# Optimization experiments

Measured on AMD Instinct MI355X. Metric: run time of the kernel, lower is better.

Reference implementation:

```python
import jax, jax.numpy as jnp
import numpy as np

Q = 4          # num_quantizers
K = 2048       # codebook_size
D = 256        # dim
B, N = 8, 8192 # batch, tokens (N % Q == 0)


def l2norm(t, eps=1e-12):
    return t / jnp.maximum(jnp.linalg.norm(t, axis=-1, keepdims=True), eps)


def setup_inputs() -> dict:
    key = jax.random.key(0)
    kx, ke = jax.random.split(key)
    x = jax.random.normal(kx, (B, N, D), dtype=jnp.float32)
    embed = jax.random.normal(ke, (Q, K, D), dtype=jnp.float32)
    return {"x": x, "embed": embed}


def reference(x, embed):
    b, n, d = x.shape
    q = embed.shape[0]
    m = n // q  # tokens per quantizer chunk
    # chunk along token axis (dim=1), as torch.chunk(x, Q, dim=1)
    xc = x.reshape(b, q, m, d).transpose(1, 0, 2, 3)  # [Q, B, M, D]

    def one_vq(xq, eq):
        # xq: [B, M, D], eq: [K, D]
        xn = l2norm(xq)
        en = l2norm(eq)
        dist = jnp.einsum('bmd,kd->bmk', xn, en)   # cosine similarity
        ind = jnp.argmax(dist, axis=-1)            # temp=0 gumbel -> argmax
        quant = eq[ind]                            # F.embedding with raw embed
        return quant, ind

    quant_c, ind_c = jax.vmap(one_vq)(xc, embed)   # [Q,B,M,D], [Q,B,M]
    quantized = quant_c.transpose(1, 0, 2, 3).reshape(b, n, d)
    encoding = ind_c.transpose(1, 0, 2).reshape(b, n)
    # eval mode: loss is sum of Q zero tensors of shape [1]
    vq_loss = jnp.zeros((1,), dtype=x.dtype)
    return quantized, encoding, vq_loss
```

## Files before the change

kernel.cpp:

```cpp
#include <hip/hip_runtime.h>
#include <math.h>

#define Bq 8
#define Nq 8192
#define Dq 256
#define Qq 4
#define Kq 2048
#define Mq (Nq / Qq)
#define TT (Bq * Nq)
#define QUANT_ELEMS ((size_t)TT * Dq)

#define CAP1Q 4096
#define THRESH 3e-4f
#define CAND_MAX 16

#define WS_CNT_OFF    0u
#define WS_LIST_OFF   1024u
#define WS_SX_OFF     66560u
#define WS_ENH_OFF    1377280u
#define WS_ENP_OFF    5571584u
#define WS_PART_OFF   13960192u

typedef __attribute__((ext_vector_type(8))) _Float16 f16x8;
typedef __attribute__((ext_vector_type(4))) _Float16 f16x4;
typedef __attribute__((ext_vector_type(4))) float    f32x4;

__device__ __forceinline__ void async_load16(const void* g, void* s) {
    __builtin_amdgcn_global_load_lds(
        (const __attribute__((address_space(1))) void*)g,
        (__attribute__((address_space(3))) void*)s, 16, 0, 0);
}

__device__ __forceinline__ float f32_div(float a, float b) {
    return (float)((double)a / (double)b);
}

__device__ __forceinline__ float np_norm_wave(const float* __restrict__ src, int ln) {
#pragma clang fp contract(off)
    float r = 0.0f;
    if (ln < 16) {
        const float* p = src + (ln >> 3) * 128 + (ln & 7);
        #pragma unroll
        for (int m = 0; m < 16; ++m) { float v = p[m * 8]; r = r + v * v; }
    }
    float t = r + __shfl_xor(r, 1, 64);
    t = t + __shfl_xor(t, 2, 64);
    t = t + __shfl_xor(t, 4, 64);
    float b0 = __shfl(t, 0, 64);
    float b1 = __shfl(t, 8, 64);
    float n2 = b0 + b1;
    return fmaxf((float)sqrt((double)n2), 1e-12f);
}

__global__ __launch_bounds__(256) void prep_kernel(const float* __restrict__ embed,
                                                   const float* __restrict__ x,
                                                   char* __restrict__ enh,
                                                   float* __restrict__ enp,
                                                   float* __restrict__ sxa,
                                                   int* __restrict__ cnt,
                                                   float* __restrict__ out) {
    if (blockIdx.x >= 2048) {
        const int tid = threadIdx.x;
        const int qd  = tid & 3;
        const int row = (blockIdx.x - 2048) * 64 + (tid >> 2);
        const float* xr = x + (size_t)row * Dq + qd * 8;
        float s2 = 0.f;
        #pragma unroll
        for (int ch = 0; ch < 8; ++ch) {
            float4 u = *(const float4*)(xr + ch * 32);
            float4 v = *(const float4*)(xr + ch * 32 + 4);
            s2 += u.x * u.x + u.y * u.y + u.z * u.z + u.w * u.w;
            s2 += v.x * v.x + v.y * v.y + v.z * v.z + v.w * v.w;
        }
        s2 += __shfl_xor(s2, 1, 64);
        s2 += __shfl_xor(s2, 2, 64);
        float sxv = 1.0f / fmaxf(sqrtf(s2), 1e-12f);
        if (qd == 0) sxa[row] = sxv;
        return;
    }

    if (blockIdx.x == 0) {
        if (threadIdx.x < 4) cnt[threadIdx.x] = 0;
        if (threadIdx.x == 0) out[QUANT_ELEMS + TT] = 0.0f;
    }

    int row = blockIdx.x * 4 + (threadIdx.x >> 6);
    int ln  = threadIdx.x & 63;
    const float* src = embed + (size_t)row * Dq;

    float4 v = *(const float4*)(src + ln * 4);
    float s = v.x * v.x + v.y * v.y + v.z * v.z + v.w * v.w;
    #pragma unroll
    for (int m = 1; m < 64; m <<= 1) s += __shfl_xor(s, m, 64);
    float sx = 1.0f / fmaxf(sqrtf(s), 1e-12f);
    int q = row >> 11, k = row & 2047, Tb = k >> 5, c = k & 31;
    int g = ln >> 1, h = ln & 1;
    f16x4 o;
    o[0] = (_Float16)(v.x * sx); o[1] = (_Float16)(v.y * sx);
    o[2] = (_Float16)(v.z * sx); o[3] = (_Float16)(v.w * sx);
    char* dst = enh + ((size_t)(q * 64 + Tb)) * 16384 + c * 512 + ((g ^ c) << 4) + h * 8;
    *(f16x4*)dst = o;

    float nm = np_norm_wave(src, ln);
    float* dstp = enp + (size_t)row * Dq;
    #pragma unroll
    for (int e = 0; e < 4; ++e) dstp[ln * 4 + e] = f32_div(src[ln * 4 + e], nm);
}

__global__ __launch_bounds__(256, 2) void gemm_kernel(const float* __restrict__ x,
                                                      const float* __restrict__ sxa,
                                                      const char* __restrict__ enh,
                                                      float4* __restrict__ part) {
    __shared__ __align__(16) char es[3][16384];

    const int tid = threadIdx.x;
    const int wv  = tid >> 6;
    const int ln  = tid & 63;
    const int qd  = ln >> 4;
    const int l15 = ln & 15;

    const int bid = blockIdx.x;
    const int h   = bid & 1;
    const int g   = bid >> 1;
    const int b   = g >> 5;
    const int rem = g & 31;
    const int q   = rem >> 3;
    const int m0  = (rem & 7) << 8;
    const int t0  = b * Nq + q * Mq + m0;
    const int t0w = t0 + wv * 64;

    f16x8 ah[4][8];
    #pragma unroll
    for (int mf = 0; mf < 4; ++mf) {
        const int tok = t0w + mf * 16 + l15;
        const float sxv = sxa[tok];
        const float* xr = x + (size_t)tok * Dq + qd * 8;
        #pragma unroll
        for (int ch = 0; ch < 8; ++ch) {
            float4 u = *(const float4*)(xr + ch * 32);
            float4 v = *(const float4*)(xr + ch * 32 + 4);
            f16x8 f;
            f[0] = (_Float16)(u.x * sxv); f[1] = (_Float16)(u.y * sxv);
            f[2] = (_Float16)(u.z * sxv); f[3] = (_Float16)(u.w * sxv);
            f[4] = (_Float16)(v.x * sxv); f[5] = (_Float16)(v.y * sxv);
            f[6] = (_Float16)(v.z * sxv); f[7] = (_Float16)(v.w * sxv);
            ah[mf][ch] = f;
        }
    }

    const char* ebase = enh + ((size_t)(q * 64 + h * 32)) * 16384;
    const int off0 = wv * 1024 + ln * 16;

    __builtin_amdgcn_sched_barrier(0);
    asm volatile("s_waitcnt vmcnt(0)");
    __builtin_amdgcn_sched_barrier(0);
    #pragma unroll
    for (int i = 0; i < 4; ++i)
        async_load16(ebase + i * 4096 + off0, es[0] + i * 4096 + off0);
    #pragma unroll
    for (int i = 0; i < 4; ++i)
        async_load16(ebase + 16384 + i * 4096 + off0, es[1] + i * 4096 + off0);
    __builtin_amdgcn_sched_barrier(0);

    float b1[4][4], b2[4][4];
    int   ic[4][4];
    #pragma unroll
    for (int mf = 0; mf < 4; ++mf)
        #pragma unroll
        for (int r = 0; r < 4; ++r) { b1[mf][r] = -2.0f; b2[mf][r] = -2.0f; ic[mf][r] = 0; }

    int rb = 0;
    for (int T = 0; T < 32; ++T) {
        if (T < 31) asm volatile("s_waitcnt vmcnt(4)");
        else        asm volatile("s_waitcnt vmcnt(0)");
        __builtin_amdgcn_sched_barrier(0);
        __builtin_amdgcn_s_barrier();
        __builtin_amdgcn_sched_barrier(0);

        if (T + 2 < 32) {
            int wb = rb + 2; if (wb >= 3) wb -= 3;
            const char* src = ebase + (size_t)(T + 2) * 16384;
            #pragma unroll
            for (int i = 0; i < 4; ++i)
                async_load16(src + i * 4096 + off0, es[wb] + i * 4096 + off0);
        }
        __builtin_amdgcn_sched_barrier(0);

        const char* esb = es[rb];

        #pragma unroll
        for (int s = 0; s < 2; ++s) {
            const int  c  = s * 16 + l15;
            const char* cb = esb + c * 512;
            f16x8 bfr[8];
            #pragma unroll
            for (int ch = 0; ch < 8; ++ch)
                bfr[ch] = *(const f16x8*)(cb + ((((ch << 2) | qd) ^ c) << 4));

            f32x4 a[4];
            #pragma unroll
            for (int mf = 0; mf < 4; ++mf) a[mf] = (f32x4){0.f, 0.f, 0.f, 0.f};
            #pragma unroll
            for (int ch = 0; ch < 8; ++ch) {
                #pragma unroll
                for (int mf = 0; mf < 4; ++mf)
                    a[mf] = __builtin_amdgcn_mfma_f32_16x16x32_f16(ah[mf][ch], bfr[ch], a[mf], 0, 0, 0);
            }

            const int cg = (h << 10) | (T << 5) | (s << 4) | l15;
            #pragma unroll
            for (int mf = 0; mf < 4; ++mf)
                #pragma unroll
                for (int r = 0; r < 4; ++r) {
                    float sv = a[mf][r];
                    bool  gt = sv > b1[mf][r];
                    b2[mf][r] = __builtin_amdgcn_fmed3f(sv, b1[mf][r], b2[mf][r]);
                    b1[mf][r] = fmaxf(b1[mf][r], sv);
                    ic[mf][r] = gt ? cg : ic[mf][r];
                }
        }
        if (++rb == 3) rb = 0;
    }

    float fb1[4][4], fb2[4][4];
    int   fic[4][4];
    #pragma unroll
    for (int mf = 0; mf < 4; ++mf)
        #pragma unroll
        for (int r = 0; r < 4; ++r) {
            float v1 = b1[mf][r], v2 = b2[mf][r]; int vi = ic[mf][r];
            #pragma unroll
            for (int m = 1; m < 16; m <<= 1) {
                float o1 = __shfl_xor(v1, m, 64);
                float o2 = __shfl_xor(v2, m, 64);
                int   oi = __shfl_xor(vi, m, 64);
                if (o1 > v1 || (o1 == v1 && oi < vi)) { v2 = fmaxf(v1, o2); v1 = o1; vi = oi; }
                else v2 = fmaxf(v2, o1);
            }
            fb1[mf][r] = v1; fb2[mf][r] = v2; fic[mf][r] = vi;
        }

    if (l15 == 0) {
        #pragma unroll
        for (int mf = 0; mf < 4; ++mf)
            #pragma unroll
            for (int r = 0; r < 4; ++r) {
                int t = t0w + mf * 16 + qd * 4 + r;
                float4 pv;
                pv.x = fb1[mf][r];
                pv.y = fb2[mf][r];
                pv.z = __int_as_float(fic[mf][r]);
                pv.w = 0.f;
                part[(size_t)h * TT + t] = pv;
            }
    }
}

__global__ __launch_bounds__(256) void merge_kernel(const float* __restrict__ embed,
                                                    const float4* __restrict__ part,
                                                    float* __restrict__ out,
                                                    int* __restrict__ cnt,
                                                    int* __restrict__ list) {
    const int wv = threadIdx.x >> 6, ln = threadIdx.x & 63;
    const int nw = gridDim.x * 4;

    for (int t = blockIdx.x * 4 + wv; t < TT; t += nw) {
        float4 pa = part[t];
        float4 pb = part[TT + t];
        float v1, v2; int vi;
        if (pb.x > pa.x) { v1 = pb.x; vi = __float_as_int(pb.z); v2 = fmaxf(pa.x, pb.y); }
        else             { v1 = pa.x; vi = __float_as_int(pa.z); v2 = fmaxf(pb.x, pa.y); }
        const int q = (t >> 11) & 3;

        int inlist = 0;
        if (ln == 0) {
            if (v1 - v2 < THRESH) {
                int pos = atomicAdd(&cnt[q], 1);
                if (pos < CAP1Q) { list[q * CAP1Q + pos] = t; inlist = 1; }
            }
            if (!inlist) out[QUANT_ELEMS + (size_t)t] = (float)vi;
        }
        inlist = __shfl(inlist, 0, 64);
        if (!inlist) {
            const float* er = embed + ((size_t)(q * Kq + vi)) * Dq;
            float4 v = *(const float4*)(er + ln * 4);
            *(float4*)(out + (size_t)t * Dq + ln * 4) = v;
        }
    }
}

__global__ __launch_bounds__(256) void cand_kernel(const float* __restrict__ x,
                                                   const float* __restrict__ sxa,
                                                   const char* __restrict__ enh,
                                                   const float* __restrict__ enp,
                                                   const float4* __restrict__ part,
                                                   const float* __restrict__ embed,
                                                   const int* __restrict__ cnt,
                                                   const int* __restrict__ list,
                                                   float* __restrict__ out) {
#pragma clang fp contract(off)
    __shared__ float xn[16][Dq];
    __shared__ int   stok[16];
    __shared__ float sv1[16];
    __shared__ int   scnt[16];
    __shared__ unsigned short scand[16][CAND_MAX];
    __shared__ float sc_s[256];
    __shared__ int   sc_c[256];
    __shared__ int   fbc[16];

    const int tid = threadIdx.x;
    const int wv  = tid >> 6;
    const int ln  = tid & 63;
    const int qd  = ln >> 4;
    const int l15 = ln & 15;

    int cq[4], nbq[4], total = 0;
    #pragma unroll
    for (int q = 0; q < 4; ++q) {
        int c = cnt[q]; if (c > CAP1Q) c = CAP1Q;
        cq[q] = c; nbq[q] = (c + 15) >> 4; total += nbq[q];
    }

    for (int j = blockIdx.x; j < total; j += gridDim.x) {
        int rem = j, q = 0;
        while (rem >= nbq[q]) { rem -= nbq[q]; ++q; }
        const int base = rem << 4;

        if (tid < 16) {
            int idx = base + tid;
            int tok = list[q * CAP1Q + (idx < cq[q] ? idx : base)];
            stok[tid] = tok;
            scnt[tid] = 0;
            sv1[tid]  = fmaxf(part[tok].x, part[TT + tok].x);
        }
        __syncthreads();

        f16x8 ah[8];
        {
            const int tok = stok[l15];
            const float sxv = sxa[tok];
            const float* xr = x + (size_t)tok * Dq + qd * 8;
            #pragma unroll
            for (int ch = 0; ch < 8; ++ch) {
                float4 u = *(const float4*)(xr + ch * 32);
                float4 v = *(const float4*)(xr + ch * 32 + 4);
                f16x8 f;
                f[0] = (_Float16)(u.x * sxv); f[1] = (_Float16)(u.y * sxv);
                f[2] = (_Float16)(u.z * sxv); f[3] = (_Float16)(u.w * sxv);
                f[4] = (_Float16)(v.x * sxv); f[5] = (_Float16)(v.y * sxv);
                f[6] = (_Float16)(v.z * sxv); f[7] = (_Float16)(v.w * sxv);
                ah[ch] = f;
            }
        }
        float thr[4];
        #pragma unroll
        for (int r = 0; r < 4; ++r) thr[r] = sv1[qd * 4 + r] - THRESH;

        const char* qbase = enh + ((size_t)(q * 64)) * 16384;
        for (int tt = 0; tt < 16; ++tt) {
            const int T = wv * 16 + tt;
            const char* tb = qbase + (size_t)T * 16384;
            #pragma unroll
            for (int s = 0; s < 2; ++s) {
                const int  c  = s * 16 + l15;
                const char* cb = tb + c * 512;
                f16x8 bfr[8];
                #pragma unroll
                for (int ch = 0; ch < 8; ++ch)
                    bfr[ch] = *(const f16x8*)(cb + ((((ch << 2) | qd) ^ c) << 4));

                f32x4 a = {0.f, 0.f, 0.f, 0.f};
                #pragma unroll
                for (int ch = 0; ch < 8; ++ch)
                    a = __builtin_amdgcn_mfma_f32_16x16x32_f16(ah[ch], bfr[ch], a, 0, 0, 0);

                const int cg = (T << 5) | (s << 4) | l15;
                #pragma unroll
                for (int r = 0; r < 4; ++r) {
                    if (a[r] >= thr[r]) {
                        int slot = qd * 4 + r;
                        int pos = atomicAdd(&scnt[slot], 1);
                        if (pos < CAND_MAX) scand[slot][pos] = (unsigned short)cg;
                    }
                }
            }
        }
        __syncthreads();

        for (int rr = 0; rr < 4; ++rr) {
            int i = wv * 4 + rr;
            const float* xr = x + (size_t)stok[i] * Dq;
            float nm = np_norm_wave(xr, ln);
            #pragma unroll
            for (int e = 0; e < 4; ++e)
                xn[i][ln * 4 + e] = f32_div(xr[ln * 4 + e], nm);
        }
        __syncthreads();

        {
            const int i = tid >> 4, sl = tid & 15;
            const int nc = scnt[i];
            float bs = -2.0f; int bc = 0x7fffffff;
            if (nc <= CAND_MAX && sl < nc) {
                int code = scand[i][sl];
                const float* er2 = enp + ((size_t)(q * Kq + code)) * Dq;
                float l0 = 0.f, l1 = 0.f, l2 = 0.f, l3 = 0.f;
                for (int d = 0; d < Dq; d += 4) {
                    float4 e = *(const float4*)(er2 + d);
                    float4 xv = *(const float4*)&xn[i][d];
                    l0 = l0 + xv.x * e.x; l1 = l1 + xv.y * e.y;
                    l2 = l2 + xv.z * e.z; l3 = l3 + xv.w * e.w;
                }
                bs = (l0 + l1) + (l2 + l3);
                bc = code;
            }
            sc_s[tid] = bs; sc_c[tid] = bc;
        }
        __syncthreads();
        if (tid < 16) {
            float bs = sc_s[tid * 16]; int bc = sc_c[tid * 16];
            #pragma unroll
            for (int sl = 1; sl < 16; ++sl) {
                float os = sc_s[tid * 16 + sl]; int oc = sc_c[tid * 16 + sl];
                if (os > bs || (os == bs && oc < bc)) { bs = os; bc = oc; }
            }
            fbc[tid] = bc;
        }
        __syncthreads();

        for (int i = 0; i < 16; ++i) {
            if (scnt[i] > CAND_MAX) {
                float bs = -2.0f; int bc = 0x7fffffff;
                for (int k = 0; k < 8; ++k) {
                    int code = k * 256 + tid;
                    const float* er2 = enp + ((size_t)(q * Kq + code)) * Dq;
                    float l0 = 0.f, l1 = 0.f, l2 = 0.f, l3 = 0.f;
                    for (int d = 0; d < Dq; d += 4) {
                        float4 e = *(const float4*)(er2 + d);
                        float4 xv = *(const float4*)&xn[i][d];
                        l0 = l0 + xv.x * e.x; l1 = l1 + xv.y * e.y;
                        l2 = l2 + xv.z * e.z; l3 = l3 + xv.w * e.w;
                    }
                    float sE = (l0 + l1) + (l2 + l3);
                    if (sE > bs || (sE == bs && code < bc)) { bs = sE; bc = code; }
                }
                sc_s[tid] = bs; sc_c[tid] = bc;
                __syncthreads();
                if (tid == 0) {
                    for (int t2 = 1; t2 < 256; ++t2) {
                        float os = sc_s[t2]; int oc = sc_c[t2];
                        if (os > bs || (os == bs && oc < bc)) { bs = os; bc = oc; }
                    }
                    fbc[i] = bc;
                }
                __syncthreads();
            }
        }

        for (int rr = 0; rr < 4; ++rr) {
            const int i = wv * 4 + rr;
            const int tok = stok[i];
            const int bc = fbc[i];
            if (ln == 0) out[QUANT_ELEMS + (size_t)tok] = (float)bc;
            const float* er = embed + ((size_t)(q * Kq + bc)) * Dq;
            float4 v = *(const float4*)(er + ln * 4);
            *(float4*)(out + (size_t)tok * Dq + ln * 4) = v;
        }
        __syncthreads();
    }
}

extern "C" void kernel_launch(void* const* d_in, const int* in_sizes, int n_in,
                              void* d_out, int out_size, void* d_ws, size_t ws_size,
                              hipStream_t stream) {
    const float* x     = (const float*)d_in[0];
    const float* embed = (const float*)d_in[1];
    float* out = (float*)d_out;
    char*  ws  = (char*)d_ws;
    int*    cnt    = (int*)(ws + WS_CNT_OFF);
    int*    list   = (int*)(ws + WS_LIST_OFF);
    float*  sxa    = (float*)(ws + WS_SX_OFF);
    char*   enh    = ws + WS_ENH_OFF;
    float*  enp    = (float*)(ws + WS_ENP_OFF);
    float4* part   = (float4*)(ws + WS_PART_OFF);

    prep_kernel<<<3072, 256, 0, stream>>>(embed, x, enh, enp, sxa, cnt, out);
    gemm_kernel<<<512, 256, 0, stream>>>(x, sxa, enh, part);
    merge_kernel<<<2048, 256, 0, stream>>>(embed, part, out, cnt, list);
    cand_kernel<<<1024, 256, 0, stream>>>(x, sxa, enh, enp, part, embed, cnt, list, out);
}
```

Before: 279.4 us.

## Give each wave private double-buffered codebook staging to drop block barriers

Replaces the block-shared triple-buffered LDS ring, which needed an s_barrier every iteration, with per-wave private double buffers. Each wave now loads its own full copy of every 16-code half-tile. This removes inter-wave synchronization, but every wave issues the global loads for all codes, so global traffic into LDS is four times higher. LDS use grows from 48KB to 64KB per block, which may limit occupancy at two blocks per CU.

New measurement: 285.1 us. 2.0% more time.

```diff
diff --git a/kernel.cpp b/kernel.cpp
--- a/kernel.cpp
+++ b/kernel.cpp
@@ -111,7 +111,7 @@
                                                       const float* __restrict__ sxa,
                                                       const char* __restrict__ enh,
                                                       float4* __restrict__ part) {
-    __shared__ __align__(16) char es[3][16384];
+    __shared__ __align__(16) char es[4][2][8192];
 
     const int tid = threadIdx.x;
     const int wv  = tid >> 6;
@@ -149,18 +149,17 @@
     }
 
     const char* ebase = enh + ((size_t)(q * 64 + h * 32)) * 16384;
-    const int off0 = wv * 1024 + ln * 16;
-
+    char* buf0 = (char*)es[wv][0];
+    char* buf1 = (char*)es[wv][1];
+
+    asm volatile("s_waitcnt vmcnt(0)" ::: "memory");
     __builtin_amdgcn_sched_barrier(0);
-    asm volatile("s_waitcnt vmcnt(0)");
-    __builtin_amdgcn_sched_barrier(0);
-    #pragma unroll
-    for (int i = 0; i < 4; ++i)
-        async_load16(ebase + i * 4096 + off0, es[0] + i * 4096 + off0);
-    #pragma unroll
-    for (int i = 0; i < 4; ++i)
-        async_load16(ebase + 16384 + i * 4096 + off0, es[1] + i * 4096 + off0);
-    __builtin_amdgcn_sched_barrier(0);
+    #pragma unroll
+    for (int i = 0; i < 8; ++i)
+        async_load16(ebase + i * 1024 + ln * 16, buf0 + i * 1024 + ln * 16);
+    #pragma unroll
+    for (int i = 0; i < 8; ++i)
+        async_load16(ebase + 8192 + i * 1024 + ln * 16, buf1 + i * 1024 + ln * 16);
 
     float b1[4][4], b2[4][4];
     int   ic[4][4];
@@ -169,57 +168,50 @@
         #pragma unroll
         for (int r = 0; r < 4; ++r) { b1[mf][r] = -2.0f; b2[mf][r] = -2.0f; ic[mf][r] = 0; }
 
-    int rb = 0;
-    for (int T = 0; T < 32; ++T) {
-        if (T < 31) asm volatile("s_waitcnt vmcnt(4)");
-        else        asm volatile("s_waitcnt vmcnt(0)");
+    for (int T = 0; T < 64; ++T) {
+        if (T < 63) asm volatile("s_waitcnt vmcnt(8)" ::: "memory");
+        else        asm volatile("s_waitcnt vmcnt(0)" ::: "memory");
         __builtin_amdgcn_sched_barrier(0);
-        __builtin_amdgcn_s_barrier();
+
+        char* mybuf = (T & 1) ? buf1 : buf0;
+        const char* cb = mybuf + l15 * 512;
+        const int   c5 = ((T & 1) << 4) | l15;
+        f16x8 bfr[8];
+        #pragma unroll
+        for (int ch = 0; ch < 8; ++ch)
+            bfr[ch] = *(const f16x8*)(cb + ((((ch << 2) | qd) ^ c5) << 4));
+
+        asm volatile("s_waitcnt lgkmcnt(0)" ::: "memory");
         __builtin_amdgcn_sched_barrier(0);
 
-        if (T + 2 < 32) {
-            int wb = rb + 2; if (wb >= 3) wb -= 3;
-            const char* src = ebase + (size_t)(T + 2) * 16384;
-            #pragma unroll
-            for (int i = 0; i < 4; ++i)
-                async_load16(src + i * 4096 + off0, es[wb] + i * 4096 + off0);
-        }
-        __builtin_amdgcn_sched_barrier(0);
-
-        const char* esb = es[rb];
-
-        #pragma unroll
-        for (int s = 0; s < 2; ++s) {
-            const int  c  = s * 16 + l15;
-            const char* cb = esb + c * 512;
-            f16x8 bfr[8];
-            #pragma unroll
-            for (int ch = 0; ch < 8; ++ch)
-                bfr[ch] = *(const f16x8*)(cb + ((((ch << 2) | qd) ^ c) << 4));
-
-            f32x4 a[4];
-            #pragma unroll
-            for (int mf = 0; mf < 4; ++mf) a[mf] = (f32x4){0.f, 0.f, 0.f, 0.f};
-            #pragma unroll
-            for (int ch = 0; ch < 8; ++ch) {
-                #pragma unroll
-                for (int mf = 0; mf < 4; ++mf)
-                    a[mf] = __builtin_amdgcn_mfma_f32_16x16x32_f16(ah[mf][ch], bfr[ch], a[mf], 0, 0, 0);
-            }
-
-            const int cg = (h << 10) | (T << 5) | (s << 4) | l15;
+        if (T + 2 < 64) {
+            const char* src = ebase + (size_t)(T + 2) * 8192;
+            #pragma unroll
+            for (int i = 0; i < 8; ++i)
+                async_load16(src + i * 1024 + ln * 16, mybuf + i * 1024 + ln * 16);
+        }
+
+        f32x4 a[4];
+        #pragma unroll
+        for (int mf = 0; mf < 4; ++mf) a[mf] = (f32x4){0.f, 0.f, 0.f, 0.f};
+        #pragma unroll
+        for (int ch = 0; ch < 8; ++ch) {
             #pragma unroll
             for (int mf = 0; mf < 4; ++mf)
-                #pragma unroll
-                for (int r = 0; r < 4; ++r) {
-                    float sv = a[mf][r];
-                    bool  gt = sv > b1[mf][r];
-                    b2[mf][r] = __builtin_amdgcn_fmed3f(sv, b1[mf][r], b2[mf][r]);
-                    b1[mf][r] = fmaxf(b1[mf][r], sv);
-                    ic[mf][r] = gt ? cg : ic[mf][r];
-                }
-        }
-        if (++rb == 3) rb = 0;
+                a[mf] = __builtin_amdgcn_mfma_f32_16x16x32_f16(ah[mf][ch], bfr[ch], a[mf], 0, 0, 0);
+        }
+
+        const int cg = (h << 10) | (T << 4) | l15;
+        #pragma unroll
+        for (int mf = 0; mf < 4; ++mf)
+            #pragma unroll
+            for (int r = 0; r < 4; ++r) {
+                float sv = a[mf][r];
+                bool  gt = sv > b1[mf][r];
+                b2[mf][r] = __builtin_amdgcn_fmed3f(sv, b1[mf][r], b2[mf][r]);
+                b1[mf][r] = fmaxf(b1[mf][r], sv);
+                ic[mf][r] = gt ? cg : ic[mf][r];
+            }
     }
 
     float fb1[4][4], fb2[4][4];
```
